# Performance work log

Hardware: AMD Instinct MI355X
Metric: run time of the kernel (lower is better)

Reference implementation:

```python
import jax, jax.numpy as jnp
import numpy as np

N, E, H, L, R, NG = 8192, 131072, 256, 3, 128, 64
NUM_ELEMENTS = 80
CUTOFF = 12.0
INV_SQRT_2 = 1.0 / np.sqrt(2.0)
INV_SQRT_3 = 1.0 / np.sqrt(3.0)
INV_SQRT_H = 1.0 / np.sqrt(H)


def _glorot(key, shape):
    fan_in, fan_out = shape[-2], shape[-1]
    return jax.random.normal(key, shape, jnp.float32) * np.sqrt(2.0 / (fan_in + fan_out))


def setup_inputs():
    key = jax.random.key(0)
    ks = jax.random.split(key, 24)
    pos = jax.random.normal(ks[0], (N, 3), jnp.float32) * 5.0
    z = jax.random.randint(ks[1], (N,), 0, NUM_ELEMENTS)
    src = jax.random.randint(ks[2], (E,), 0, N)
    off = jax.random.randint(ks[3], (E,), 1, N)
    dst = (src + off) % N  # guarantee no self-loops (dist > 0)
    edge_index = jnp.stack([src, dst])
    batch = jnp.sort(jax.random.randint(ks[4], (N,), 0, NG))
    return {
        "pos": pos,
        "atom_emb": jax.random.normal(ks[5], (NUM_ELEMENTS, H), jnp.float32),
        "ln_w": jnp.ones((L, H), jnp.float32),
        "ln_b": jnp.zeros((L, H), jnp.float32),
        "xp_w1": _glorot(ks[6], (L, H, H)),
        "xp_b1": jnp.zeros((L, H), jnp.float32),
        "xp_w2": _glorot(ks[7], (L, H, 3 * H)),
        "xp_b2": jnp.zeros((L, 3 * H), jnp.float32),
        "rbf_w": _glorot(ks[8], (L, R, 3 * H)),
        "rbf_b": jnp.zeros((L, 3 * H), jnp.float32),
        "vec_w": _glorot(ks[9], (L, H, 2 * H)),
        "xv_w1": _glorot(ks[10], (L, 2 * H, H)),
        "xv_b1": jnp.zeros((L, H), jnp.float32),
        "xv_w2": _glorot(ks[11], (L, H, 3 * H)),
        "xv_b2": jnp.zeros((L, 3 * H), jnp.float32),
        "oe_w1": _glorot(ks[12], (H, H // 2)),
        "oe_b1": jnp.zeros((H // 2,), jnp.float32),
        "oe_w2": _glorot(ks[13], (H // 2, 1)),
        "oe_b2": jnp.zeros((1,), jnp.float32),
        "z": z,
        "edge_index": edge_index,
        "batch": batch,
    }


def _gaussian_rbf(dist):
    offset = jnp.linspace(0.0, CUTOFF, R)
    coeff = -0.5 / (offset[1] - offset[0]) ** 2
    return jnp.exp(coeff * (dist[:, None] - offset[None, :]) ** 2)  # [E, R]


def _layernorm(x, w, b):
    mu = x.mean(-1, keepdims=True)
    var = x.var(-1, keepdims=True)
    return (x - mu) / jnp.sqrt(var + 1e-5) * w + b


def reference(pos, atom_emb, ln_w, ln_b, xp_w1, xp_b1, xp_w2, xp_b2,
              rbf_w, rbf_b, vec_w, xv_w1, xv_b1, xv_w2, xv_b2,
              oe_w1, oe_b1, oe_w2, oe_b2, z, edge_index, batch):
    src, dst = edge_index[0], edge_index[1]
    rel = pos[src] - pos[dst]                       # [E, 3]
    dist = jnp.sqrt((rel ** 2).sum(-1))             # [E]
    edge_rbf = _gaussian_rbf(dist)                  # [E, R]
    edge_vector = rel / dist[:, None]               # [E, 3] unit vectors

    x = atom_emb[z]                                 # [N, H]
    vec = jnp.zeros((N, 3, H), x.dtype)

    for l in range(L):
        # ---- PaiNNMessage ----
        xh = _layernorm(x, ln_w[l], ln_b[l])
        xh = jax.nn.silu(xh @ xp_w1[l] + xp_b1[l]) @ xp_w2[l] + xp_b2[l]  # [N, 3H]
        rbfh = edge_rbf @ rbf_w[l] + rbf_b[l]                             # [E, 3H]
        m = xh[src] * rbfh
        mx, xh2, xh3 = jnp.split(m, 3, axis=-1)
        xh2 = xh2 * INV_SQRT_3
        mvec = (vec[src] * xh2[:, None, :] + xh3[:, None, :] * edge_vector[:, :, None]) * INV_SQRT_H
        dx = jax.ops.segment_sum(mx, dst, num_segments=N)
        dvec = jax.ops.segment_sum(mvec, dst, num_segments=N)
        x = (x + dx) * INV_SQRT_2
        vec = vec + dvec

        # ---- PaiNNUpdate ----
        vp = vec @ vec_w[l]                          # [N, 3, 2H]
        vec1, vec2 = jnp.split(vp, 2, axis=-1)
        vec_dot = (vec1 * vec2).sum(axis=1) * INV_SQRT_H           # [N, H]
        vnorm = jnp.sqrt((vec2 ** 2).sum(axis=1) + 1e-8)           # [N, H]
        h = jnp.concatenate([x, vnorm], axis=-1)
        h = jax.nn.silu(h @ xv_w1[l] + xv_b1[l]) @ xv_w2[l] + xv_b2[l]
        xv1, xv2, xv3 = jnp.split(h, 3, axis=-1)
        dx = (xv1 + xv2 * vec_dot) * INV_SQRT_2
        dvec = xv3[:, None, :] * vec1
        x = (x + dx) * INV_SQRT_2
        vec = vec + dvec

    # ---- energy head: per-atom MLP then per-molecule sum ----
    per_atom = jax.nn.silu(x @ oe_w1 + oe_b1) @ oe_w2 + oe_b2      # [N, 1]
    energy = jax.ops.segment_sum(per_atom, batch, num_segments=NG)  # [NG, 1]
    return energy
```

## Files before the change

### kernel.cpp

```cpp
#include <hip/hip_runtime.h>
#include <hip/hip_bf16.h>
#include <math.h>

#define NN 8192
#define EE 131072
#define HH 256
#define LL 3
#define RR 128
#define NGG 64
#define MSG_WAVES 8

typedef __attribute__((ext_vector_type(8))) short bf16x8;
typedef __attribute__((ext_vector_type(4))) float f32x4;
typedef unsigned short u16;

#if defined(__has_builtin)
#if __has_builtin(__builtin_amdgcn_fdot2_f32_bf16)
#define HAVE_FDOT2 1
typedef __attribute__((ext_vector_type(2))) __bf16 bf16x2_t;
union BU { unsigned u; bf16x2_t v; };
#endif
#if __has_builtin(__builtin_amdgcn_global_load_lds)
#define HAVE_GLL 1
#endif
#endif

union U4 { ushort4 v; unsigned short a[4]; };
union U8 { uint4 v; unsigned short a[8]; unsigned w[4]; };

__device__ __forceinline__ float silu(float v) { return v / (1.0f + expf(-v)); }
__device__ __forceinline__ float b2f(unsigned short u) { return __uint_as_float(((unsigned)u) << 16); }
__device__ __forceinline__ unsigned short f2b(float f) {
    unsigned u = __float_as_uint(f);
    u += 0x7fff + ((u >> 16) & 1);
    return (unsigned short)(u >> 16);
}

constexpr float kInvSqrt2 = 0.70710678118654752440f;
constexpr float kInvSqrt3 = 0.57735026918962576451f;
constexpr float kInvSqrtH = 0.0625f;

__global__ void k_zero(float* __restrict__ p, int n4) {
    int i = blockIdx.x * 256 + threadIdx.x;
    if (i < n4) ((float4*)p)[i] = make_float4(0.f, 0.f, 0.f, 0.f);
}

__global__ __launch_bounds__(256) void k_wt_all(
    const float* __restrict__ xp_w1, const float* __restrict__ xp_w2,
    const float* __restrict__ rbf_w, const float* __restrict__ vec_w,
    const float* __restrict__ xv_w1, const float* __restrict__ xv_w2,
    const float* __restrict__ oe_w1,
    u16* __restrict__ xp_w1T, u16* __restrict__ xp_w2T, u16* __restrict__ rbf_wP,
    u16* __restrict__ vec_wT, u16* __restrict__ xv_w1T, u16* __restrict__ xv_w2T,
    u16* __restrict__ oe_w1T) {
    int bid = blockIdx.x;
    const float* src; u16* dst; int K, N, t, pairmode = 0;
    if (bid < 2400) {
        int l = bid / 800, r = bid % 800;
        if (r < 64)       { src = xp_w1 + (size_t)l * 65536;  dst = xp_w1T + (size_t)l * 65536;  K = 256; N = 256; t = r; }
        else if (r < 256) { src = xp_w2 + (size_t)l * 196608; dst = xp_w2T + (size_t)l * 196608; K = 256; N = 768; t = r - 64; }
        else if (r < 352) { src = rbf_w + (size_t)l * 98304;  dst = rbf_wP + (size_t)l * 98304;  K = 128; N = 768; t = r - 256; pairmode = 1; }
        else if (r < 480) { src = vec_w + (size_t)l * 131072; dst = vec_wT + (size_t)l * 131072; K = 256; N = 512; t = r - 352; }
        else if (r < 608) { src = xv_w1 + (size_t)l * 131072; dst = xv_w1T + (size_t)l * 131072; K = 512; N = 256; t = r - 480; }
        else              { src = xv_w2 + (size_t)l * 196608; dst = xv_w2T + (size_t)l * 196608; K = 256; N = 768; t = r - 608; }
    } else {
        src = oe_w1; dst = oe_w1T; K = 256; N = 128; t = bid - 2400;
    }
    int nx = N >> 5;
    int bn = (t % nx) * 32, bk = (t / nx) * 32;
    int tx = threadIdx.x & 31, ty = threadIdx.x >> 5;
    if (pairmode) {
#pragma unroll
        for (int i = 0; i < 32; i += 8) {
            int k = bk + ty + i, n = bn + tx;
            dst[(size_t)(k >> 1) * 1536 + n * 2 + (k & 1)] = f2b(src[(size_t)k * N + n]);
        }
        return;
    }
    __shared__ float tile[32][33];
#pragma unroll
    for (int i = 0; i < 32; i += 8)
        tile[ty + i][tx] = src[(size_t)(bk + ty + i) * N + bn + tx];
    __syncthreads();
#pragma unroll
    for (int i = 0; i < 32; i += 8)
        dst[(size_t)(bn + ty + i) * K + bk + tx] = f2b(tile[tx][ty + i]);
}

__global__ void k_init_ln(const float* __restrict__ emb, const int* __restrict__ z,
                          const float* __restrict__ w, const float* __restrict__ b,
                          float* __restrict__ x, u16* __restrict__ xlnb) {
    int n = blockIdx.x, t = threadIdx.x;
    float v = emb[z[n] * HH + t];
    x[(size_t)n * HH + t] = v;
    float s = v, q = v * v;
#pragma unroll
    for (int m = 32; m >= 1; m >>= 1) {
        s += __shfl_xor(s, m, 64);
        q += __shfl_xor(q, m, 64);
    }
    __shared__ float s_sum[4], s_sq[4];
    int wid = t >> 6;
    if ((t & 63) == 0) { s_sum[wid] = s; s_sq[wid] = q; }
    __syncthreads();
    float S = s_sum[0] + s_sum[1] + s_sum[2] + s_sum[3];
    float Q = s_sq[0] + s_sq[1] + s_sq[2] + s_sq[3];
    float mu = S * (1.0f / HH);
    float var = Q * (1.0f / HH) - mu * mu;
    float rs = rsqrtf(var + 1e-5f);
    xlnb[(size_t)n * HH + t] = f2b((v - mu) * rs * w[t] + b[t]);
}

__global__ void k_geom_hist(const float* __restrict__ pos, const int* __restrict__ ei,
                            float* __restrict__ ev, int* __restrict__ deg) {
    int e = blockIdx.x * 256 + threadIdx.x;
    if (e >= EE) return;
    int s = ei[e], d = ei[EE + e];
    float rx = pos[s * 3 + 0] - pos[d * 3 + 0];
    float ry = pos[s * 3 + 1] - pos[d * 3 + 1];
    float rz = pos[s * 3 + 2] - pos[d * 3 + 2];
    float dist = sqrtf(rx * rx + ry * ry + rz * rz);
    float inv = 1.0f / dist;
    ((float4*)ev)[e] = make_float4(rx * inv, ry * inv, rz * inv, dist);
    atomicAdd(&deg[d], 1);
}

__global__ void k_scan1(const int* __restrict__ deg, int* __restrict__ row_ptr,
                        int* __restrict__ csum) {
    __shared__ int buf[256];
    int t = threadIdx.x, base = blockIdx.x * 256;
    int v = deg[base + t];
    buf[t] = v;
    __syncthreads();
    for (int ofs = 1; ofs < 256; ofs <<= 1) {
        int add = (t >= ofs) ? buf[t - ofs] : 0;
        __syncthreads();
        buf[t] += add;
        __syncthreads();
    }
    row_ptr[base + t] = buf[t] - v;
    if (t == 255) csum[blockIdx.x] = buf[t];
}
__global__ void k_scan2(int* __restrict__ csum) {
    if (threadIdx.x == 0) {
        int acc = 0;
        for (int i = 0; i < 32; ++i) { int v = csum[i]; csum[i] = acc; acc += v; }
        csum[32] = acc;
    }
}
__global__ void k_scan3(const int* __restrict__ csum, int* __restrict__ row_ptr,
                        int* __restrict__ fill) {
    int i = blockIdx.x * 256 + threadIdx.x;
    int v = row_ptr[i] + csum[i >> 8];
    row_ptr[i] = v;
    fill[i] = v;
    if (i == 0) row_ptr[NN] = csum[32];
}

__global__ void k_sort(const int* __restrict__ deg, int* __restrict__ dorder) {
    __shared__ int bins[256];
    __shared__ int base[256];
    int t = threadIdx.x;
    bins[t] = 0;
    __syncthreads();
    for (int d = t; d < NN; d += 256) {
        int b = deg[d]; b = b > 255 ? 255 : b;
        atomicAdd(&bins[b], 1);
    }
    __syncthreads();
    if (t == 0) {
        int acc = 0;
        for (int k = 255; k >= 0; --k) { base[k] = acc; acc += bins[k]; }
    }
    __syncthreads();
    bins[t] = 0;
    __syncthreads();
    for (int d = t; d < NN; d += 256) {
        int b = deg[d]; b = b > 255 ? 255 : b;
        int p = atomicAdd(&bins[b], 1);
        dorder[base[b] + p] = d;
    }
}

__global__ void k_scatter(const int* __restrict__ ei, const float* __restrict__ ev,
                          int* __restrict__ fill, int* __restrict__ srcp,
                          float4* __restrict__ evp, int* __restrict__ kptab,
                          unsigned* __restrict__ gtab) {
    int e = blockIdx.x * 256 + threadIdx.x;
    if (e >= EE) return;
    int d = ei[EE + e];
    int pos = atomicAdd(&fill[d], 1);
    float4 e4 = ((const float4*)ev)[e];
    srcp[pos] = ei[e];
    evp[pos] = e4;
    const float step = 12.0f / 127.0f;
    const float coeff = -0.5f / (step * step);
    float dist = e4.w;
    int k0 = ((int)floorf(dist / step) - 3) & ~1;
    k0 = k0 < 0 ? 0 : (k0 > 120 ? 120 : k0);
    float g[8];
#pragma unroll
    for (int k = 0; k < 8; ++k) {
        float t = dist - (k0 + k) * step;
        g[k] = expf(coeff * t * t);
    }
    kptab[pos] = k0 >> 1;
    unsigned g0 = (unsigned)f2b(g[0]) | ((unsigned)f2b(g[1]) << 16);
    unsigned g1 = (unsigned)f2b(g[2]) | ((unsigned)f2b(g[3]) << 16);
    unsigned g2 = (unsigned)f2b(g[4]) | ((unsigned)f2b(g[5]) << 16);
    unsigned g3 = (unsigned)f2b(g[6]) | ((unsigned)f2b(g[7]) << 16);
    ((uint4*)gtab)[pos] = make_uint4(g0, g1, g2, g3);
}

template <int OUT_BF16, int ACT, int TM, int TN>
__global__ __launch_bounds__(256) void k_gemm(
    const u16* __restrict__ A, const u16* __restrict__ BT,
    const float* __restrict__ bias, void* __restrict__ C, int M, int K, int N) {
    __shared__ u16 As[TM * 64];
    __shared__ u16 Bs[TN * 64];
    const int MI = TM / 32;
    const int NJ = TN / 32;
    int tid = threadIdx.x;
    int wave = tid >> 6, lane = tid & 63;
    int bm = blockIdx.y * TM, bn = blockIdx.x * TN;
    int wm = (wave & 1) * (TM / 2), wn = (wave >> 1) * (TN / 2);
    int lm = lane & 15;
    int kg = lane >> 4;
    f32x4 acc[MI][NJ] = {};

    for (int k0 = 0; k0 < K; k0 += 64) {
#pragma unroll
        for (int it = 0; it < TM / 32; ++it) {
            int idx = it * 256 + tid;
            int r = idx >> 3, seg = idx & 7;
#ifdef HAVE_GLL
            __builtin_amdgcn_global_load_lds(
                (const unsigned*)&A[(size_t)(bm + r) * K + k0 + seg * 8],
                (unsigned*)&As[idx * 8], 16, 0, 0);
#else
            *(uint4*)&As[idx * 8] = *(const uint4*)&A[(size_t)(bm + r) * K + k0 + seg * 8];
#endif
        }
#pragma unroll
        for (int it = 0; it < TN / 32; ++it) {
            int idx = it * 256 + tid;
            int r = idx >> 3, seg = idx & 7;
#ifdef HAVE_GLL
            __builtin_amdgcn_global_load_lds(
                (const unsigned*)&BT[(size_t)(bn + r) * K + k0 + seg * 8],
                (unsigned*)&Bs[idx * 8], 16, 0, 0);
#else
            *(uint4*)&Bs[idx * 8] = *(const uint4*)&BT[(size_t)(bn + r) * K + k0 + seg * 8];
#endif
        }
        __syncthreads();
#pragma unroll
        for (int kh = 0; kh < 2; ++kh) {
            bf16x8 af[MI], bfr[NJ];
#pragma unroll
            for (int i = 0; i < MI; ++i)
                af[i] = *(const bf16x8*)&As[(wm + i * 16 + lm) * 64 + kh * 32 + kg * 8];
#pragma unroll
            for (int j = 0; j < NJ; ++j)
                bfr[j] = *(const bf16x8*)&Bs[(wn + j * 16 + lm) * 64 + kh * 32 + kg * 8];
#pragma unroll
            for (int i = 0; i < MI; ++i)
#pragma unroll
                for (int j = 0; j < NJ; ++j)
                    acc[i][j] = __builtin_amdgcn_mfma_f32_16x16x32_bf16(af[i], bfr[j], acc[i][j], 0, 0, 0);
        }
        __syncthreads();
    }

#pragma unroll
    for (int j = 0; j < NJ; ++j) {
        int col = bn + wn + j * 16 + lm;
        float bv = bias ? bias[col] : 0.f;
#pragma unroll
        for (int i = 0; i < MI; ++i) {
            int row0 = bm + wm + i * 16 + kg * 4;
#pragma unroll
            for (int r = 0; r < 4; ++r) {
                float v = acc[i][j][r] + bv;
                if (ACT) v = silu(v);
                if (OUT_BF16)
                    ((u16*)C)[(size_t)(row0 + r) * N + col] = f2b(v);
                else
                    ((float*)C)[(size_t)(row0 + r) * N + col] = v;
            }
        }
    }
}

__global__ __launch_bounds__(512) void k_msg(
    const u16* __restrict__ xhb, const u16* __restrict__ vinb,
    const int* __restrict__ srcp, const float4* __restrict__ evp,
    const int* __restrict__ row_ptr, const int* __restrict__ kptab,
    const unsigned* __restrict__ gtab, const u16* __restrict__ WP ,
    const float* __restrict__ rbias, float* __restrict__ x,
    const float* __restrict__ vin, u16* __restrict__ vecMb,
    const int* __restrict__ dorder) {
    __shared__ u16 Wp[64 * 512];
    int tid = threadIdx.x;
    int wave = tid >> 6, lane = tid & 63;
    int c0 = lane * 4;
    int d = dorder[blockIdx.x * MSG_WAVES + wave];
    int E0 = row_ptr[d], E1 = row_ptr[d + 1];
    float accv[3][4] = {};

#pragma unroll
    for (int p = 0; p < 3; ++p) {
        __syncthreads();
#pragma unroll
        for (int it = 0; it < 8; ++it) {
            int idx = it * 512 + tid;
            int r = idx >> 6;
            int c8 = (idx & 63) * 8;
            *(uint4*)&Wp[r * 512 + c8] =
                *(const uint4*)&WP[(size_t)r * 1536 + p * 512 + c8];
        }
        __syncthreads();
        float4 bb = ((const float4*)(rbias + p * 256))[lane];
        float bias4[4] = {bb.x, bb.y, bb.z, bb.w};
        float accx[4] = {};

        int kp_n = 0; uint4 gt_n = make_uint4(0, 0, 0, 0);
        U4 X_n; U4 V0_n, V1_n, V2_n; float4 ev_n;
        X_n.v = make_ushort4(0, 0, 0, 0);
        V0_n = X_n; V1_n = X_n; V2_n = X_n;
        ev_n = make_float4(0.f, 0.f, 0.f, 0.f);
        if (E0 < E1) {
            int s0 = srcp[E0];
            kp_n = kptab[E0];
            gt_n = ((const uint4*)gtab)[E0];
            X_n.v = *(const ushort4*)(xhb + (size_t)s0 * 768 + p * 256 + c0);
            if (p == 1) {
                V0_n.v = *(const ushort4*)(vinb + (size_t)s0 * 768 + c0);
                V1_n.v = *(const ushort4*)(vinb + (size_t)s0 * 768 + 256 + c0);
                V2_n.v = *(const ushort4*)(vinb + (size_t)s0 * 768 + 512 + c0);
            }
            if (p == 2) ev_n = evp[E0];
        }
        for (int j = E0; j < E1; ++j) {
            int kp = kp_n;
            uint4 gt = gt_n;
            U4 X = X_n, V0 = V0_n, V1 = V1_n, V2 = V2_n;
            float4 ev4 = ev_n;
            if (j + 1 < E1) {
                int s2 = srcp[j + 1];
                kp_n = kptab[j + 1];
                gt_n = ((const uint4*)gtab)[j + 1];
                X_n.v = *(const ushort4*)(xhb + (size_t)s2 * 768 + p * 256 + c0);
                if (p == 1) {
                    V0_n.v = *(const ushort4*)(vinb + (size_t)s2 * 768 + c0);
                    V1_n.v = *(const ushort4*)(vinb + (size_t)s2 * 768 + 256 + c0);
                    V2_n.v = *(const ushort4*)(vinb + (size_t)s2 * 768 + 512 + c0);
                }
                if (p == 2) ev_n = evp[j + 1];
            }
            unsigned gp0 = gt.x, gp1 = gt.y, gp2 = gt.z, gp3 = gt.w;
            float rr[4] = {bias4[0], bias4[1], bias4[2], bias4[3]};
            {
                U8 w0, w1, w2, w3;
                w0.v = *(const uint4*)&Wp[(kp + 0) * 512 + c0 * 2];
                w1.v = *(const uint4*)&Wp[(kp + 1) * 512 + c0 * 2];
                w2.v = *(const uint4*)&Wp[(kp + 2) * 512 + c0 * 2];
                w3.v = *(const uint4*)&Wp[(kp + 3) * 512 + c0 * 2];
#ifdef HAVE_FDOT2
                BU g0; g0.u = gp0; BU g1; g1.u = gp1;
                BU g2; g2.u = gp2; BU g3; g3.u = gp3;
#pragma unroll
                for (int c = 0; c < 4; ++c) {
                    BU a; a.u = w0.w[c];
                    rr[c] = __builtin_amdgcn_fdot2_f32_bf16(a.v, g0.v, rr[c], false);
                    a.u = w1.w[c];
                    rr[c] = __builtin_amdgcn_fdot2_f32_bf16(a.v, g1.v, rr[c], false);
                    a.u = w2.w[c];
                    rr[c] = __builtin_amdgcn_fdot2_f32_bf16(a.v, g2.v, rr[c], false);
                    a.u = w3.w[c];
                    rr[c] = __builtin_amdgcn_fdot2_f32_bf16(a.v, g3.v, rr[c], false);
                }
#else
                float ge0 = b2f((u16)(gp0 & 0xffff)), go0 = b2f((u16)(gp0 >> 16));
                float ge1 = b2f((u16)(gp1 & 0xffff)), go1 = b2f((u16)(gp1 >> 16));
                float ge2 = b2f((u16)(gp2 & 0xffff)), go2 = b2f((u16)(gp2 >> 16));
                float ge3 = b2f((u16)(gp3 & 0xffff)), go3 = b2f((u16)(gp3 >> 16));
#pragma unroll
                for (int c = 0; c < 4; ++c) {
                    rr[c] += ge0 * b2f(w0.a[2 * c]) + go0 * b2f(w0.a[2 * c + 1]);
                    rr[c] += ge1 * b2f(w1.a[2 * c]) + go1 * b2f(w1.a[2 * c + 1]);
                    rr[c] += ge2 * b2f(w2.a[2 * c]) + go2 * b2f(w2.a[2 * c + 1]);
                    rr[c] += ge3 * b2f(w3.a[2 * c]) + go3 * b2f(w3.a[2 * c + 1]);
                }
#endif
            }
            if (p == 0) {
#pragma unroll
                for (int c = 0; c < 4; ++c) accx[c] += b2f(X.a[c]) * rr[c];
            } else if (p == 1) {
#pragma unroll
                for (int c = 0; c < 4; ++c) {
                    float m1 = b2f(X.a[c]) * rr[c] * kInvSqrt3;
                    accv[0][c] += b2f(V0.a[c]) * m1;
                    accv[1][c] += b2f(V1.a[c]) * m1;
                    accv[2][c] += b2f(V2.a[c]) * m1;
                }
            } else {
#pragma unroll
                for (int c = 0; c < 4; ++c) {
                    float m2 = b2f(X.a[c]) * rr[c];
                    accv[0][c] += m2 * ev4.x;
                    accv[1][c] += m2 * ev4.y;
                    accv[2][c] += m2 * ev4.z;
                }
            }
        }
        if (p == 0) {
            size_t xi = (size_t)d * 256 + c0;
            float4 xv = *(const float4*)&x[xi];
            xv.x = (xv.x + accx[0]) * kInvSqrt2;
            xv.y = (xv.y + accx[1]) * kInvSqrt2;
            xv.z = (xv.z + accx[2]) * kInvSqrt2;
            xv.w = (xv.w + accx[3]) * kInvSqrt2;
            *(float4*)&x[xi] = xv;
        }
    }
#pragma unroll
    for (int k = 0; k < 3; ++k) {
        size_t idx = (size_t)d * 768 + k * 256 + c0;
        float4 vv = *(const float4*)&vin[idx];
        ushort4 u;
        u.x = f2b(vv.x + accv[k][0] * kInvSqrtH);
        u.y = f2b(vv.y + accv[k][1] * kInvSqrtH);
        u.z = f2b(vv.z + accv[k][2] * kInvSqrtH);
        u.w = f2b(vv.w + accv[k][3] * kInvSqrtH);
        *(ushort4*)&vecMb[idx] = u;
    }
}

__global__ void k_vecdot(const u16* __restrict__ vp, const float* __restrict__ x,
                         float* __restrict__ vec_dot, u16* __restrict__ hcat) {
    int idx = blockIdx.x * 256 + threadIdx.x;
    int n = idx >> 5, lg = idx & 31;
    int c0 = lg * 8;
    const u16* p = vp + (size_t)n * 1536;
    float ds[8] = {}, qs[8] = {};
#pragma unroll
    for (int k = 0; k < 3; ++k) {
        uint4 a = *(const uint4*)&p[k * 512 + c0];
        uint4 b = *(const uint4*)&p[k * 512 + 256 + c0];
        const unsigned* aw = (const unsigned*)&a;
        const unsigned* bw = (const unsigned*)&b;
#pragma unroll
        for (int w = 0; w < 4; ++w) {
            float a0 = __uint_as_float(aw[w] << 16);
            float a1 = __uint_as_float(aw[w] & 0xffff0000u);
            float b0 = __uint_as_float(bw[w] << 16);
            float b1 = __uint_as_float(bw[w] & 0xffff0000u);
            ds[2 * w]     += a0 * b0;  qs[2 * w]     += b0 * b0;
            ds[2 * w + 1] += a1 * b1;  qs[2 * w + 1] += b1 * b1;
        }
    }
    size_t vo = (size_t)n * 256 + c0;
    *(float4*)&vec_dot[vo] =
        make_float4(ds[0] * kInvSqrtH, ds[1] * kInvSqrtH, ds[2] * kInvSqrtH, ds[3] * kInvSqrtH);
    *(float4*)&vec_dot[vo + 4] =
        make_float4(ds[4] * kInvSqrtH, ds[5] * kInvSqrtH, ds[6] * kInvSqrtH, ds[7] * kInvSqrtH);
    float4 x0 = *(const float4*)&x[vo];
    float4 x1 = *(const float4*)&x[vo + 4];
    *(ushort4*)&hcat[(size_t)n * 512 + c0] =
        make_ushort4(f2b(x0.x), f2b(x0.y), f2b(x0.z), f2b(x0.w));
    *(ushort4*)&hcat[(size_t)n * 512 + c0 + 4] =
        make_ushort4(f2b(x1.x), f2b(x1.y), f2b(x1.z), f2b(x1.w));
    *(ushort4*)&hcat[(size_t)n * 512 + 256 + c0] =
        make_ushort4(f2b(sqrtf(qs[0] + 1e-8f)), f2b(sqrtf(qs[1] + 1e-8f)),
                     f2b(sqrtf(qs[2] + 1e-8f)), f2b(sqrtf(qs[3] + 1e-8f)));
    *(ushort4*)&hcat[(size_t)n * 512 + 256 + c0 + 4] =
        make_ushort4(f2b(sqrtf(qs[4] + 1e-8f)), f2b(sqrtf(qs[5] + 1e-8f)),
                     f2b(sqrtf(qs[6] + 1e-8f)), f2b(sqrtf(qs[7] + 1e-8f)));
}

__global__ void k_update_out(const u16* __restrict__ hout, const float* __restrict__ vec_dot,
                             const u16* __restrict__ vp, float* __restrict__ x,
                             const u16* __restrict__ vecMb, float* __restrict__ vfin,
                             u16* __restrict__ vb,
                             const float* __restrict__ lnw, const float* __restrict__ lnb,
                             u16* __restrict__ xout) {
    int idx = blockIdx.x * 256 + threadIdx.x;
    int n = idx >> 5, lg = idx & 31;
    int c0 = lg * 8;
    size_t hb = (size_t)n * 768;
    uint4 H1 = *(const uint4*)&hout[hb + c0];
    uint4 H2 = *(const uint4*)&hout[hb + 256 + c0];
    uint4 H3 = *(const uint4*)&hout[hb + 512 + c0];
    const unsigned* h1w = (const unsigned*)&H1;
    const unsigned* h2w = (const unsigned*)&H2;
    const unsigned* h3w = (const unsigned*)&H3;
    size_t xo = (size_t)n * 256 + c0;
    float4 vd0 = *(const float4*)&vec_dot[xo];
    float4 vd1 = *(const float4*)&vec_dot[xo + 4];
    float vd[8] = {vd0.x, vd0.y, vd0.z, vd0.w, vd1.x, vd1.y, vd1.z, vd1.w};
    float4 x0 = *(const float4*)&x[xo];
    float4 x1 = *(const float4*)&x[xo + 4];
    float xv[8] = {x0.x, x0.y, x0.z, x0.w, x1.x, x1.y, x1.z, x1.w};
    float nx[8], xv3[8];
#pragma unroll
    for (int w = 0; w < 4; ++w) {
        float a1 = __uint_as_float(h1w[w] << 16), b1 = __uint_as_float(h1w[w] & 0xffff0000u);
        float a2 = __uint_as_float(h2w[w] << 16), b2v = __uint_as_float(h2w[w] & 0xffff0000u);
        nx[2 * w]     = (xv[2 * w]     + (a1 + a2  * vd[2 * w])     * kInvSqrt2) * kInvSqrt2;
        nx[2 * w + 1] = (xv[2 * w + 1] + (b1 + b2v * vd[2 * w + 1]) * kInvSqrt2) * kInvSqrt2;
        xv3[2 * w]     = __uint_as_float(h3w[w] << 16);
        xv3[2 * w + 1] = __uint_as_float(h3w[w] & 0xffff0000u);
    }
    *(float4*)&x[xo]     = make_float4(nx[0], nx[1], nx[2], nx[3]);
    *(float4*)&x[xo + 4] = make_float4(nx[4], nx[5], nx[6], nx[7]);
#pragma unroll
    for (int k = 0; k < 3; ++k) {
        size_t vo = hb + k * 256 + c0;
        uint4 VM = *(const uint4*)&vecMb[vo];
        uint4 VP = *(const uint4*)&vp[(size_t)n * 1536 + k * 512 + c0];
        const unsigned* vmw = (const unsigned*)&VM;
        const unsigned* vpw = (const unsigned*)&VP;
        float nv[8];
#pragma unroll
        for (int w = 0; w < 4; ++w) {
            nv[2 * w]     = __uint_as_float(vmw[w] << 16)
                          + xv3[2 * w]     * __uint_as_float(vpw[w] << 16);
            nv[2 * w + 1] = __uint_as_float(vmw[w] & 0xffff0000u)
                          + xv3[2 * w + 1] * __uint_as_float(vpw[w] & 0xffff0000u);
        }
        *(float4*)&vfin[vo]     = make_float4(nv[0], nv[1], nv[2], nv[3]);
        *(float4*)&vfin[vo + 4] = make_float4(nv[4], nv[5], nv[6], nv[7]);
        *(ushort4*)&vb[vo]     = make_ushort4(f2b(nv[0]), f2b(nv[1]), f2b(nv[2]), f2b(nv[3]));
        *(ushort4*)&vb[vo + 4] = make_ushort4(f2b(nv[4]), f2b(nv[5]), f2b(nv[6]), f2b(nv[7]));
    }
    if (lnw) {
        float s = 0.f, q = 0.f;
#pragma unroll
        for (int c = 0; c < 8; ++c) { s += nx[c]; q += nx[c] * nx[c]; }
#pragma unroll
        for (int m = 16; m >= 1; m >>= 1) {
            s += __shfl_xor(s, m, 64);
            q += __shfl_xor(q, m, 64);
        }
        float mu = s * (1.0f / HH);
        float var = q * (1.0f / HH) - mu * mu;
        float rs = rsqrtf(var + 1e-5f);
        float4 w0 = *(const float4*)&lnw[c0], w1 = *(const float4*)&lnw[c0 + 4];
        float4 bb0 = *(const float4*)&lnb[c0], bb1 = *(const float4*)&lnb[c0 + 4];
        float lw[8] = {w0.x, w0.y, w0.z, w0.w, w1.x, w1.y, w1.z, w1.w};
        float lb[8] = {bb0.x, bb0.y, bb0.z, bb0.w, bb1.x, bb1.y, bb1.z, bb1.w};
        u16 o[8];
#pragma unroll
        for (int c = 0; c < 8; ++c) o[c] = f2b((nx[c] - mu) * rs * lw[c] + lb[c]);
        *(ushort4*)&xout[xo]     = make_ushort4(o[0], o[1], o[2], o[3]);
        *(ushort4*)&xout[xo + 4] = make_ushort4(o[4], o[5], o[6], o[7]);
    } else {
        *(ushort4*)&xout[xo]     = make_ushort4(f2b(nx[0]), f2b(nx[1]), f2b(nx[2]), f2b(nx[3]));
        *(ushort4*)&xout[xo + 4] = make_ushort4(f2b(nx[4]), f2b(nx[5]), f2b(nx[6]), f2b(nx[7]));
    }
}

__global__ void k_energy2(const float* __restrict__ h, const float* __restrict__ w2,
                          const float* __restrict__ b2, const int* __restrict__ batch,
                          float* __restrict__ out) {
    __shared__ float g[NGG];
    int t = threadIdx.x;
    if (t < NGG) g[t] = 0.f;
    __syncthreads();
    int a = blockIdx.x * 256 + t;
    const float4* hr = (const float4*)(h + (size_t)a * 128);
    const float4* w4 = (const float4*)w2;
    float acc = 0.f;
#pragma unroll 8
    for (int i = 0; i < 32; ++i) {
        float4 hv = hr[i], wv = w4[i];
        acc += hv.x * wv.x + hv.y * wv.y + hv.z * wv.z + hv.w * wv.w;
    }
    acc += b2[0];
    atomicAdd(&g[batch[a]], acc);
    __syncthreads();
    if (t < NGG && g[t] != 0.f) atomicAdd(&out[t], g[t]);
}

extern "C" void kernel_launch(void* const* d_in, const int* in_sizes, int n_in,
                              void* d_out, int out_size, void* d_ws, size_t ws_size,
                              hipStream_t stream) {
    const float* pos      = (const float*)d_in[0];
    const float* atom_emb = (const float*)d_in[1];
    const float* ln_w     = (const float*)d_in[2];
    const float* ln_b     = (const float*)d_in[3];
    const float* xp_w1    = (const float*)d_in[4];
    const float* xp_b1    = (const float*)d_in[5];
    const float* xp_w2    = (const float*)d_in[6];
    const float* xp_b2    = (const float*)d_in[7];
    const float* rbf_w    = (const float*)d_in[8];
    const float* rbf_b    = (const float*)d_in[9];
    const float* vec_w    = (const float*)d_in[10];
    const float* xv_w1    = (const float*)d_in[11];
    const float* xv_b1    = (const float*)d_in[12];
    const float* xv_w2    = (const float*)d_in[13];
    const float* xv_b2    = (const float*)d_in[14];
    const float* oe_w1    = (const float*)d_in[15];
    const float* oe_b1    = (const float*)d_in[16];
    const float* oe_w2    = (const float*)d_in[17];
    const float* oe_b2    = (const float*)d_in[18];
    const int*   z        = (const int*)d_in[19];
    const int*   ei       = (const int*)d_in[20];
    const int*   batch    = (const int*)d_in[21];
    float* out = (float*)d_out;

    char* ws = (char*)d_ws;
    size_t off = 0;
    auto alloc = [&](size_t b) {
        void* p = ws + off;
        off = (off + b + 255) & ~(size_t)255;
        return p;
    };
    float*    x      = (float*)alloc((size_t)NN * HH * 4);
    float*    vecA   = (float*)alloc((size_t)NN * 768 * 4);
    u16*      vb     = (u16*)alloc((size_t)NN * 768 * 2);
    u16*      vecMb  = (u16*)alloc((size_t)NN * 768 * 2);
    u16*      xlnb   = (u16*)alloc((size_t)NN * HH * 2);
    u16*      t1b    = (u16*)alloc((size_t)NN * HH * 2);
    u16*      xhb    = (u16*)alloc((size_t)NN * 768 * 2);
    float*    vdot   = (float*)alloc((size_t)NN * HH * 4);
    u16*      vpb    = (u16*)alloc((size_t)NN * 1536 * 2);
    u16*      houtb  = (u16*)alloc((size_t)NN * 768 * 2);
    float*    ev     = (float*)alloc((size_t)EE * 4 * 4);
    int*      deg    = (int*)alloc((size_t)NN * 4);
    int*      row_ptr= (int*)alloc((size_t)(NN + 1) * 4);
    int*      fill   = (int*)alloc((size_t)NN * 4);
    int*      dorder = (int*)alloc((size_t)NN * 4);
    int*      csum   = (int*)alloc((size_t)33 * 4);
    int*      srcp   = (int*)alloc((size_t)EE * 4);
    float4*   evp    = (float4*)alloc((size_t)EE * 16);
    int*      kptab  = (int*)alloc((size_t)EE * 4);
    unsigned* gtab   = (unsigned*)alloc((size_t)EE * 16);
    u16* xp_w1T   = (u16*)alloc((size_t)3 * 256 * 256 * 2);
    u16* xp_w2T   = (u16*)alloc((size_t)3 * 768 * 256 * 2);
    u16* rbf_wP   = (u16*)alloc((size_t)3 * 128 * 768 * 2);
    u16* vec_wT   = (u16*)alloc((size_t)3 * 512 * 256 * 2);
    u16* xv_w1T   = (u16*)alloc((size_t)3 * 256 * 512 * 2);
    u16* xv_w2T   = (u16*)alloc((size_t)3 * 768 * 256 * 2);
    u16* oe_w1T   = (u16*)alloc((size_t)128 * 256 * 2);
    (void)ws_size;

    u16*   h1b   = t1b;
    u16*   hcatb = xhb;
    float* heng  = vdot;
    u16*   xb    = xlnb;

    k_wt_all<<<2432, 256, 0, stream>>>(xp_w1, xp_w2, rbf_w, vec_w, xv_w1, xv_w2, oe_w1,
                                       xp_w1T, xp_w2T, rbf_wP, vec_wT, xv_w1T, xv_w2T, oe_w1T);
    k_zero<<<(36 * 1024 * 1024 / 16 + 255) / 256, 256, 0, stream>>>(vecA, 36 * 1024 * 1024 / 16);
    k_zero<<<8, 256, 0, stream>>>((float*)deg, NN / 4);
    k_init_ln<<<NN, 256, 0, stream>>>(atom_emb, z, ln_w, ln_b, x, xlnb);
    k_geom_hist<<<EE / 256, 256, 0, stream>>>(pos, ei, ev, deg);
    k_scan1<<<32, 256, 0, stream>>>(deg, row_ptr, csum);
    k_scan2<<<1, 64, 0, stream>>>(csum);
    k_scan3<<<32, 256, 0, stream>>>(csum, row_ptr, fill);
    k_sort<<<1, 256, 0, stream>>>(deg, dorder);
    k_scatter<<<EE / 256, 256, 0, stream>>>(ei, ev, fill, srcp, evp, kptab, gtab);

    for (int l = 0; l < LL; ++l) {
        k_gemm<1, 1, 32, 64><<<dim3(4, NN / 32), 256, 0, stream>>>(
            xlnb, xp_w1T + (size_t)l * 256 * 256, xp_b1 + l * HH, t1b, NN, 256, 256);
        k_gemm<1, 0, 32, 128><<<dim3(6, NN / 32), 256, 0, stream>>>(
            t1b, xp_w2T + (size_t)l * 768 * 256, xp_b2 + l * 768, xhb, NN, 256, 768);
        k_msg<<<NN / MSG_WAVES, 64 * MSG_WAVES, 0, stream>>>(
            xhb, vb, srcp, evp, row_ptr, kptab, gtab,
            rbf_wP + (size_t)l * 128 * 768, rbf_b + l * 768, x, vecA, vecMb, dorder);

        k_gemm<1, 0, 64, 128><<<dim3(4, 3 * NN / 64), 256, 0, stream>>>(
            vecMb, vec_wT + (size_t)l * 512 * 256, nullptr, vpb, 3 * NN, 256, 512);
        k_vecdot<<<NN / 8, 256, 0, stream>>>(vpb, x, vdot, hcatb);
        k_gemm<1, 1, 32, 64><<<dim3(4, NN / 32), 256, 0, stream>>>(
            hcatb, xv_w1T + (size_t)l * 256 * 512, xv_b1 + l * HH, h1b, NN, 512, 256);
        k_gemm<1, 0, 32, 128><<<dim3(6, NN / 32), 256, 0, stream>>>(
            h1b, xv_w2T + (size_t)l * 768 * 256, xv_b2 + l * 768, houtb, NN, 256, 768);
        bool last = (l == LL - 1);
        k_update_out<<<NN / 8, 256, 0, stream>>>(
            houtb, vdot, vpb, x, vecMb, vecA, vb,
            last ? nullptr : ln_w + (l + 1) * HH,
            last ? nullptr : ln_b + (l + 1) * HH, xlnb);
    }

    k_gemm<0, 1, 32, 64><<<dim3(2, NN / 32), 256, 0, stream>>>(
        xb, oe_w1T, oe_b1, heng, NN, 256, 128);
    k_zero<<<1, 256, 0, stream>>>(out, NGG / 4);
    k_energy2<<<32, 256, 0, stream>>>(heng, oe_w2, oe_b2, batch, out);
}
```

Measured before the change: 709.2 us.

## Fuse three message-kernel passes into one edge loop reading RBF weights from global

```diff
diff --git a/kernel.cpp b/kernel.cpp
--- a/kernel.cpp
+++ b/kernel.cpp
@@ -8,7 +8,6 @@
 #define LL 3
 #define RR 128
 #define NGG 64
-#define MSG_WAVES 8
 
 typedef __attribute__((ext_vector_type(8))) short bf16x8;
 typedef __attribute__((ext_vector_type(4))) float f32x4;
@@ -292,7 +291,7 @@
     }
 }
 
-__global__ __launch_bounds__(512) void k_msg(
+__global__ __launch_bounds__(256) void k_msg(
     const u16* __restrict__ xhb, const u16* __restrict__ vinb,
     const int* __restrict__ srcp, const float4* __restrict__ evp,
     const int* __restrict__ row_ptr, const int* __restrict__ kptab,
@@ -300,130 +299,108 @@
     const float* __restrict__ rbias, float* __restrict__ x,
     const float* __restrict__ vin, u16* __restrict__ vecMb,
     const int* __restrict__ dorder) {
-    __shared__ u16 Wp[64 * 512];
     int tid = threadIdx.x;
     int wave = tid >> 6, lane = tid & 63;
     int c0 = lane * 4;
-    int d = dorder[blockIdx.x * MSG_WAVES + wave];
+    int d = dorder[blockIdx.x * 4 + wave];
     int E0 = row_ptr[d], E1 = row_ptr[d + 1];
+    float4 bb0 = ((const float4*)rbias)[lane];
+    float4 bb1 = ((const float4*)(rbias + 256))[lane];
+    float4 bb2 = ((const float4*)(rbias + 512))[lane];
+    float accx[4] = {};
     float accv[3][4] = {};
 
-#pragma unroll
-    for (int p = 0; p < 3; ++p) {
-        __syncthreads();
-#pragma unroll
-        for (int it = 0; it < 8; ++it) {
-            int idx = it * 512 + tid;
-            int r = idx >> 6;
-            int c8 = (idx & 63) * 8;
-            *(uint4*)&Wp[r * 512 + c8] =
-                *(const uint4*)&WP[(size_t)r * 1536 + p * 512 + c8];
-        }
-        __syncthreads();
-        float4 bb = ((const float4*)(rbias + p * 256))[lane];
-        float bias4[4] = {bb.x, bb.y, bb.z, bb.w};
-        float accx[4] = {};
-
-        int kp_n = 0; uint4 gt_n = make_uint4(0, 0, 0, 0);
-        U4 X_n; U4 V0_n, V1_n, V2_n; float4 ev_n;
-        X_n.v = make_ushort4(0, 0, 0, 0);
-        V0_n = X_n; V1_n = X_n; V2_n = X_n;
-        ev_n = make_float4(0.f, 0.f, 0.f, 0.f);
-        if (E0 < E1) {
-            int s0 = srcp[E0];
-            kp_n = kptab[E0];
-            gt_n = ((const uint4*)gtab)[E0];
-            X_n.v = *(const ushort4*)(xhb + (size_t)s0 * 768 + p * 256 + c0);
-            if (p == 1) {
-                V0_n.v = *(const ushort4*)(vinb + (size_t)s0 * 768 + c0);
-                V1_n.v = *(const ushort4*)(vinb + (size_t)s0 * 768 + 256 + c0);
-                V2_n.v = *(const ushort4*)(vinb + (size_t)s0 * 768 + 512 + c0);
+    for (int j = E0; j < E1; ++j) {
+        int s = srcp[j];
+        int kp = kptab[j];
+        uint4 gt = ((const uint4*)gtab)[j];
+        float4 ev4 = evp[j];
+        const u16* wb = WP + (size_t)kp * 1536 + c0 * 2;
+        U8 w00, w01, w02, w10, w11, w12, w20, w21, w22, w30, w31, w32;
+        w00.v = *(const uint4*)&wb[0];
+        w01.v = *(const uint4*)&wb[512];
+        w02.v = *(const uint4*)&wb[1024];
+        w10.v = *(const uint4*)&wb[1536];
+        w11.v = *(const uint4*)&wb[2048];
+        w12.v = *(const uint4*)&wb[2560];
+        w20.v = *(const uint4*)&wb[3072];
+        w21.v = *(const uint4*)&wb[3584];
+        w22.v = *(const uint4*)&wb[4096];
+        w30.v = *(const uint4*)&wb[4608];
+        w31.v = *(const uint4*)&wb[5120];
+        w32.v = *(const uint4*)&wb[5632];
+        const u16* xr = xhb + (size_t)s * 768 + c0;
+        const u16* vr = vinb + (size_t)s * 768 + c0;
+        U4 X0, X1, X2, V0, V1, V2;
+        X0.v = *(const ushort4*)(xr);
+        X1.v = *(const ushort4*)(xr + 256);
+        X2.v = *(const ushort4*)(xr + 512);
+        V0.v = *(const ushort4*)(vr);
+        V1.v = *(const ushort4*)(vr + 256);
+        V2.v = *(const ushort4*)(vr + 512);
+        float rr0[4] = {bb0.x, bb0.y, bb0.z, bb0.w};
+        float rr1[4] = {bb1.x, bb1.y, bb1.z, bb1.w};
+        float rr2[4] = {bb2.x, bb2.y, bb2.z, bb2.w};
+#ifdef HAVE_FDOT2
+        BU g0; g0.u = gt.x; BU g1; g1.u = gt.y;
+        BU g2; g2.u = gt.z; BU g3; g3.u = gt.w;
+#pragma unroll
+        for (int c = 0; c < 4; ++c) {
+            BU a;
+            a.u = w00.w[c]; rr0[c] = __builtin_amdgcn_fdot2_f32_bf16(a.v, g0.v, rr0[c], false);
+            a.u = w10.w[c]; rr0[c] = __builtin_amdgcn_fdot2_f32_bf16(a.v, g1.v, rr0[c], false);
+            a.u = w20.w[c]; rr0[c] = __builtin_amdgcn_fdot2_f32_bf16(a.v, g2.v, rr0[c], false);
+            a.u = w30.w[c]; rr0[c] = __builtin_amdgcn_fdot2_f32_bf16(a.v, g3.v, rr0[c], false);
+            a.u = w01.w[c]; rr1[c] = __builtin_amdgcn_fdot2_f32_bf16(a.v, g0.v, rr1[c], false);
+            a.u = w11.w[c]; rr1[c] = __builtin_amdgcn_fdot2_f32_bf16(a.v, g1.v, rr1[c], false);
+            a.u = w21.w[c]; rr1[c] = __builtin_amdgcn_fdot2_f32_bf16(a.v, g2.v, rr1[c], false);
+            a.u = w31.w[c]; rr1[c] = __builtin_amdgcn_fdot2_f32_bf16(a.v, g3.v, rr1[c], false);
+            a.u = w02.w[c]; rr2[c] = __builtin_amdgcn_fdot2_f32_bf16(a.v, g0.v, rr2[c], false);
+            a.u = w12.w[c]; rr2[c] = __builtin_amdgcn_fdot2_f32_bf16(a.v, g1.v, rr2[c], false);
+            a.u = w22.w[c]; rr2[c] = __builtin_amdgcn_fdot2_f32_bf16(a.v, g2.v, rr2[c], false);
+            a.u = w32.w[c]; rr2[c] = __builtin_amdgcn_fdot2_f32_bf16(a.v, g3.v, rr2[c], false);
+        }
+#else
+        {
+            float ge0 = b2f((u16)(gt.x & 0xffff)), go0 = b2f((u16)(gt.x >> 16));
+            float ge1 = b2f((u16)(gt.y & 0xffff)), go1 = b2f((u16)(gt.y >> 16));
+            float ge2 = b2f((u16)(gt.z & 0xffff)), go2 = b2f((u16)(gt.z >> 16));
+            float ge3 = b2f((u16)(gt.w & 0xffff)), go3 = b2f((u16)(gt.w >> 16));
+#pragma unroll
+            for (int c = 0; c < 4; ++c) {
+                rr0[c] += ge0 * b2f(w00.a[2 * c]) + go0 * b2f(w00.a[2 * c + 1])
+                        + ge1 * b2f(w10.a[2 * c]) + go1 * b2f(w10.a[2 * c + 1])
+                        + ge2 * b2f(w20.a[2 * c]) + go2 * b2f(w20.a[2 * c + 1])
+                        + ge3 * b2f(w30.a[2 * c]) + go3 * b2f(w30.a[2 * c + 1]);
+                rr1[c] += ge0 * b2f(w01.a[2 * c]) + go0 * b2f(w01.a[2 * c + 1])
+                        + ge1 * b2f(w11.a[2 * c]) + go1 * b2f(w11.a[2 * c + 1])
+                        + ge2 * b2f(w21.a[2 * c]) + go2 * b2f(w21.a[2 * c + 1])
+                        + ge3 * b2f(w31.a[2 * c]) + go3 * b2f(w31.a[2 * c + 1]);
+                rr2[c] += ge0 * b2f(w02.a[2 * c]) + go0 * b2f(w02.a[2 * c + 1])
+                        + ge1 * b2f(w12.a[2 * c]) + go1 * b2f(w12.a[2 * c + 1])
+                        + ge2 * b2f(w22.a[2 * c]) + go2 * b2f(w22.a[2 * c + 1])
+                        + ge3 * b2f(w32.a[2 * c]) + go3 * b2f(w32.a[2 * c + 1]);
             }
-            if (p == 2) ev_n = evp[E0];
-        }
-        for (int j = E0; j < E1; ++j) {
-            int kp = kp_n;
-            uint4 gt = gt_n;
-            U4 X = X_n, V0 = V0_n, V1 = V1_n, V2 = V2_n;
-            float4 ev4 = ev_n;
-            if (j + 1 < E1) {
-                int s2 = srcp[j + 1];
-                kp_n = kptab[j + 1];
-                gt_n = ((const uint4*)gtab)[j + 1];
-                X_n.v = *(const ushort4*)(xhb + (size_t)s2 * 768 + p * 256 + c0);
-                if (p == 1) {
-                    V0_n.v = *(const ushort4*)(vinb + (size_t)s2 * 768 + c0);
-                    V1_n.v = *(const ushort4*)(vinb + (size_t)s2 * 768 + 256 + c0);
-                    V2_n.v = *(const ushort4*)(vinb + (size_t)s2 * 768 + 512 + c0);
-                }
-                if (p == 2) ev_n = evp[j + 1];
-            }
-            unsigned gp0 = gt.x, gp1 = gt.y, gp2 = gt.z, gp3 = gt.w;
-            float rr[4] = {bias4[0], bias4[1], bias4[2], bias4[3]};
-            {
-                U8 w0, w1, w2, w3;
-                w0.v = *(const uint4*)&Wp[(kp + 0) * 512 + c0 * 2];
-                w1.v = *(const uint4*)&Wp[(kp + 1) * 512 + c0 * 2];
-                w2.v = *(const uint4*)&Wp[(kp + 2) * 512 + c0 * 2];
-                w3.v = *(const uint4*)&Wp[(kp + 3) * 512 + c0 * 2];
-#ifdef HAVE_FDOT2
-                BU g0; g0.u = gp0; BU g1; g1.u = gp1;
-                BU g2; g2.u = gp2; BU g3; g3.u = gp3;
-#pragma unroll
-                for (int c = 0; c < 4; ++c) {
-                    BU a; a.u = w0.w[c];
-                    rr[c] = __builtin_amdgcn_fdot2_f32_bf16(a.v, g0.v, rr[c], false);
-                    a.u = w1.w[c];
-                    rr[c] = __builtin_amdgcn_fdot2_f32_bf16(a.v, g1.v, rr[c], false);
-                    a.u = w2.w[c];
-                    rr[c] = __builtin_amdgcn_fdot2_f32_bf16(a.v, g2.v, rr[c], false);
-                    a.u = w3.w[c];
-                    rr[c] = __builtin_amdgcn_fdot2_f32_bf16(a.v, g3.v, rr[c], false);
-                }
-#else
-                float ge0 = b2f((u16)(gp0 & 0xffff)), go0 = b2f((u16)(gp0 >> 16));
-                float ge1 = b2f((u16)(gp1 & 0xffff)), go1 = b2f((u16)(gp1 >> 16));
-                float ge2 = b2f((u16)(gp2 & 0xffff)), go2 = b2f((u16)(gp2 >> 16));
-                float ge3 = b2f((u16)(gp3 & 0xffff)), go3 = b2f((u16)(gp3 >> 16));
-#pragma unroll
-                for (int c = 0; c < 4; ++c) {
-                    rr[c] += ge0 * b2f(w0.a[2 * c]) + go0 * b2f(w0.a[2 * c + 1]);
-                    rr[c] += ge1 * b2f(w1.a[2 * c]) + go1 * b2f(w1.a[2 * c + 1]);
-                    rr[c] += ge2 * b2f(w2.a[2 * c]) + go2 * b2f(w2.a[2 * c + 1]);
-                    rr[c] += ge3 * b2f(w3.a[2 * c]) + go3 * b2f(w3.a[2 * c + 1]);
-                }
+        }
 #endif
-            }
-            if (p == 0) {
-#pragma unroll
-                for (int c = 0; c < 4; ++c) accx[c] += b2f(X.a[c]) * rr[c];
-            } else if (p == 1) {
-#pragma unroll
-                for (int c = 0; c < 4; ++c) {
-                    float m1 = b2f(X.a[c]) * rr[c] * kInvSqrt3;
-                    accv[0][c] += b2f(V0.a[c]) * m1;
-                    accv[1][c] += b2f(V1.a[c]) * m1;
-                    accv[2][c] += b2f(V2.a[c]) * m1;
-                }
-            } else {
-#pragma unroll
-                for (int c = 0; c < 4; ++c) {
-                    float m2 = b2f(X.a[c]) * rr[c];
-                    accv[0][c] += m2 * ev4.x;
-                    accv[1][c] += m2 * ev4.y;
-                    accv[2][c] += m2 * ev4.z;
-                }
-            }
-        }
-        if (p == 0) {
-            size_t xi = (size_t)d * 256 + c0;
-            float4 xv = *(const float4*)&x[xi];
-            xv.x = (xv.x + accx[0]) * kInvSqrt2;
-            xv.y = (xv.y + accx[1]) * kInvSqrt2;
-            xv.z = (xv.z + accx[2]) * kInvSqrt2;
-            xv.w = (xv.w + accx[3]) * kInvSqrt2;
-            *(float4*)&x[xi] = xv;
-        }
+#pragma unroll
+        for (int c = 0; c < 4; ++c) {
+            accx[c] += b2f(X0.a[c]) * rr0[c];
+            float m1 = b2f(X1.a[c]) * rr1[c] * kInvSqrt3;
+            float m2 = b2f(X2.a[c]) * rr2[c];
+            accv[0][c] += b2f(V0.a[c]) * m1 + m2 * ev4.x;
+            accv[1][c] += b2f(V1.a[c]) * m1 + m2 * ev4.y;
+            accv[2][c] += b2f(V2.a[c]) * m1 + m2 * ev4.z;
+        }
+    }
+    {
+        size_t xi = (size_t)d * 256 + c0;
+        float4 xv = *(const float4*)&x[xi];
+        xv.x = (xv.x + accx[0]) * kInvSqrt2;
+        xv.y = (xv.y + accx[1]) * kInvSqrt2;
+        xv.z = (xv.z + accx[2]) * kInvSqrt2;
+        xv.w = (xv.w + accx[3]) * kInvSqrt2;
+        *(float4*)&x[xi] = xv;
     }
 #pragma unroll
     for (int k = 0; k < 3; ++k) {
@@ -669,7 +646,7 @@
             xlnb, xp_w1T + (size_t)l * 256 * 256, xp_b1 + l * HH, t1b, NN, 256, 256);
         k_gemm<1, 0, 32, 128><<<dim3(6, NN / 32), 256, 0, stream>>>(
             t1b, xp_w2T + (size_t)l * 768 * 256, xp_b2 + l * 768, xhb, NN, 256, 768);
-        k_msg<<<NN / MSG_WAVES, 64 * MSG_WAVES, 0, stream>>>(
+        k_msg<<<NN / 4, 256, 0, stream>>>(
             xhb, vb, srcp, evp, row_ptr, kptab, gtab,
             rbf_wP + (size_t)l * 128 * 768, rbf_b + l * 768, x, vecA, vecMb, dorder);
 
```

Measured after the change: 716.4 us. No clear change (+1.0%).

## Fuse two-layer MLP GEMM pairs into a single kernel keeping hidden in LDS

Applied to the files above, without the earlier changes.

```diff
diff --git a/kernel.cpp b/kernel.cpp
--- a/kernel.cpp
+++ b/kernel.cpp
@@ -289,6 +289,58 @@
                     ((float*)C)[(size_t)(row0 + r) * N + col] = v;
             }
         }
+    }
+}
+
+template <int K1, int N2>
+__global__ __launch_bounds__(256) void k_mlp2(
+    const u16* __restrict__ A, const u16* __restrict__ B1T, const float* __restrict__ b1,
+    const u16* __restrict__ B2T, const float* __restrict__ b2, u16* __restrict__ C) {
+    __shared__ u16 Hs[16 * 256];
+    int tid = threadIdx.x;
+    int wave = tid >> 6, lane = tid & 63;
+    int lm = lane & 15, kg = lane >> 4;
+    int bm = blockIdx.x * 16;
+    f32x4 acc1[4] = {};
+    for (int kk = 0; kk < K1; kk += 32) {
+        bf16x8 af = *(const bf16x8*)&A[(size_t)(bm + lm) * K1 + kk + kg * 8];
+#pragma unroll
+        for (int j = 0; j < 4; ++j) {
+            bf16x8 bf = *(const bf16x8*)&B1T[(size_t)(wave * 64 + j * 16 + lm) * K1 + kk + kg * 8];
+            acc1[j] = __builtin_amdgcn_mfma_f32_16x16x32_bf16(af, bf, acc1[j], 0, 0, 0);
+        }
+    }
+#pragma unroll
+    for (int j = 0; j < 4; ++j) {
+        int col = wave * 64 + j * 16 + lm;
+        float bv = b1[col];
+#pragma unroll
+        for (int r = 0; r < 4; ++r) {
+            int row = kg * 4 + r;
+            int byt = (row * 512 + col * 2) ^ ((row & 7) << 4);
+            *(u16*)((char*)Hs + byt) = f2b(silu(acc1[j][r] + bv));
+        }
+    }
+    __syncthreads();
+    const int NJ = N2 / 64;
+    f32x4 acc2[NJ] = {};
+    int wn = wave * (N2 / 4);
+    for (int kk = 0; kk < 256; kk += 32) {
+        int byt = (lm * 512 + (kk + kg * 8) * 2) ^ ((lm & 7) << 4);
+        bf16x8 af = *(const bf16x8*)((const char*)Hs + byt);
+#pragma unroll
+        for (int j = 0; j < NJ; ++j) {
+            bf16x8 bf = *(const bf16x8*)&B2T[(size_t)(wn + j * 16 + lm) * 256 + kk + kg * 8];
+            acc2[j] = __builtin_amdgcn_mfma_f32_16x16x32_bf16(af, bf, acc2[j], 0, 0, 0);
+        }
+    }
+#pragma unroll
+    for (int j = 0; j < NJ; ++j) {
+        int col = wn + j * 16 + lm;
+        float bv = b2[col];
+#pragma unroll
+        for (int r = 0; r < 4; ++r)
+            C[(size_t)(bm + kg * 4 + r) * N2 + col] = f2b(acc2[j][r] + bv);
     }
 }
 
@@ -646,8 +698,8 @@
     u16* xv_w2T   = (u16*)alloc((size_t)3 * 768 * 256 * 2);
     u16* oe_w1T   = (u16*)alloc((size_t)128 * 256 * 2);
     (void)ws_size;
-
-    u16*   h1b   = t1b;
+    (void)t1b;
+
     u16*   hcatb = xhb;
     float* heng  = vdot;
     u16*   xb    = xlnb;
@@ -665,10 +717,9 @@
     k_scatter<<<EE / 256, 256, 0, stream>>>(ei, ev, fill, srcp, evp, kptab, gtab);
 
     for (int l = 0; l < LL; ++l) {
-        k_gemm<1, 1, 32, 64><<<dim3(4, NN / 32), 256, 0, stream>>>(
-            xlnb, xp_w1T + (size_t)l * 256 * 256, xp_b1 + l * HH, t1b, NN, 256, 256);
-        k_gemm<1, 0, 32, 128><<<dim3(6, NN / 32), 256, 0, stream>>>(
-            t1b, xp_w2T + (size_t)l * 768 * 256, xp_b2 + l * 768, xhb, NN, 256, 768);
+        k_mlp2<256, 768><<<NN / 16, 256, 0, stream>>>(
+            xlnb, xp_w1T + (size_t)l * 256 * 256, xp_b1 + l * HH,
+            xp_w2T + (size_t)l * 768 * 256, xp_b2 + l * 768, xhb);
         k_msg<<<NN / MSG_WAVES, 64 * MSG_WAVES, 0, stream>>>(
             xhb, vb, srcp, evp, row_ptr, kptab, gtab,
             rbf_wP + (size_t)l * 128 * 768, rbf_b + l * 768, x, vecA, vecMb, dorder);
@@ -676,10 +727,9 @@
         k_gemm<1, 0, 64, 128><<<dim3(4, 3 * NN / 64), 256, 0, stream>>>(
             vecMb, vec_wT + (size_t)l * 512 * 256, nullptr, vpb, 3 * NN, 256, 512);
         k_vecdot<<<NN / 8, 256, 0, stream>>>(vpb, x, vdot, hcatb);
-        k_gemm<1, 1, 32, 64><<<dim3(4, NN / 32), 256, 0, stream>>>(
-            hcatb, xv_w1T + (size_t)l * 256 * 512, xv_b1 + l * HH, h1b, NN, 512, 256);
-        k_gemm<1, 0, 32, 128><<<dim3(6, NN / 32), 256, 0, stream>>>(
-            h1b, xv_w2T + (size_t)l * 768 * 256, xv_b2 + l * 768, houtb, NN, 256, 768);
+        k_mlp2<512, 768><<<NN / 16, 256, 0, stream>>>(
+            hcatb, xv_w1T + (size_t)l * 256 * 512, xv_b1 + l * HH,
+            xv_w2T + (size_t)l * 768 * 256, xv_b2 + l * 768, houtb);
         bool last = (l == LL - 1);
         k_update_out<<<NN / 8, 256, 0, stream>>>(
             houtb, vdot, vpb, x, vecMb, vecA, vb,
```

After: 856.3 us. 20.7% more time.
